# Optimization experiments

Measured on AMD Instinct MI355X. Metric: run time of the kernel, lower is better.

## Reference

```python
import jax, jax.numpy as jnp
import numpy as np

B, C, H, W = 4, 256, 64, 64
TOPK = 3
RAT_S = 0.05  # rat_s passed in Corr.forward


def _zero_window_mask(h, w, rat_s=RAT_S):
    # mask[m, i, j] = 1 - gaussian centered at pixel m=(m//w, m%w); sigma=(h*rat_s, w*rat_s)
    sr, sc = h * rat_s, w * rat_s
    r = jnp.arange(h, dtype=jnp.float32)
    c = jnp.arange(w, dtype=jnp.float32)
    cent_r = jnp.repeat(r, w)  # [hw]
    cent_c = jnp.tile(c, h)    # [hw]
    g = (jnp.exp(-((r[None, :, None] - cent_r[:, None, None]) ** 2) / (2.0 * sr * sr))
         * jnp.exp(-((c[None, None, :] - cent_c[:, None, None]) ** 2) / (2.0 * sc * sc)))
    return (1.0 - g).reshape(h * w, h * w)


def setup_inputs() -> dict:
    key = jax.random.key(0)
    x = jax.random.normal(key, (B, C, H, W), dtype=jnp.float32)
    alpha = jnp.asarray(5.0, dtype=jnp.float32)  # learned scalar nn.Parameter
    return {"x": x, "alpha": alpha}


def reference(x, alpha):
    b, c, h, w = x.shape
    # F.normalize(x, p=2, dim=-3): L2-normalize channels with eps clamp
    nrm = jnp.linalg.norm(x, axis=1, keepdims=True)
    xn = x / jnp.maximum(nrm, 1e-12)
    xf = xn.reshape(b, c, h * w)
    # correlation GEMM: [b, hw, hw]
    aff = jnp.einsum('bcm,bcn->bmn', xf, xf)
    aff = aff * _zero_window_mask(h, w)[None]
    s = aff * alpha
    xc = jax.nn.softmax(s, axis=-1) * jax.nn.softmax(s, axis=-2)
    # topk over the source-pixel dim (dim=-3 of [b, hw, h, w])
    xc = xc.reshape(b, h * w, h, w).transpose(0, 2, 3, 1)  # [b, h, w, hw]
    val, _ = jax.lax.top_k(xc, TOPK)                        # [b, h, w, k]
    return val.transpose(0, 3, 1, 2)                        # [b, k, h, w]
```

## Files before the change

kernel.cpp:

```cpp
#include <hip/hip_runtime.h>
#include <hip/hip_bf16.h>


#define HW 4096
#define CDIM 256
#define INV2S2 0.048828125f
#define NEGINF -1e30f
#define NTILE 528

typedef __bf16 bf16;
typedef _Float16 f16;
typedef __attribute__((ext_vector_type(8))) __bf16 bf16x8;
typedef __attribute__((ext_vector_type(4))) _Float16 f16x4;
typedef __attribute__((ext_vector_type(4))) float f32x4;

#define GAS __attribute__((address_space(1)))
#define LAS __attribute__((address_space(3)))

__device__ __forceinline__ void ins3(float v, float& t0, float& t1, float& t2) {
    float n0 = fmaxf(t0, v);
    float n1 = __builtin_amdgcn_fmed3f(t0, t1, v);
    float n2 = __builtin_amdgcn_fmed3f(t1, t2, v);
    t0 = n0; t1 = n1; t2 = n2;
}

__device__ __forceinline__ void decode_tri(int t, int& mt, int& nt) {
    int m = (int)((sqrtf(8.f * (float)t + 1.f) - 1.f) * 0.5f);
    while ((m + 1) * (m + 2) / 2 <= t) ++m;
    while (m * (m + 1) / 2 > t) --m;
    mt = m;
    nt = t - m * (m + 1) / 2;
}

__global__ __launch_bounds__(256) void corr_norm(const float* __restrict__ x,
                                                 bf16* __restrict__ xnT) {
    __shared__ float red[4][64];
    __shared__ float invn[64];
    __shared__ __align__(16) bf16 T[64][264];
    int tid = threadIdx.x;
    int pl = tid & 63, cg = tid >> 6;
    int P0 = blockIdx.x * 64;
    int P = P0 + pl;
    int b = P >> 12;
    int pix = P & 4095;
    const float* xb = x + ((size_t)(b * CDIM + cg * 64) << 12) + pix;
    float v[64];
    float ss = 0.f;
#pragma unroll
    for (int j = 0; j < 64; ++j) {
        v[j] = xb[(size_t)j << 12];
        ss += v[j] * v[j];
    }
    red[cg][pl] = ss;
    __syncthreads();
    if (tid < 64) {
        float s = red[0][tid] + red[1][tid] + red[2][tid] + red[3][tid];
        invn[tid] = 1.0f / fmaxf(sqrtf(s), 1e-12f);
    }
    __syncthreads();
    float inv = invn[pl];
#pragma unroll
    for (int j0 = 0; j0 < 64; j0 += 8) {
        bf16x8 pk;
#pragma unroll
        for (int j = 0; j < 8; ++j) pk[j] = (bf16)(v[j0 + j] * inv);
        *(bf16x8*)(&T[pl][cg * 64 + j0]) = pk;
    }
    __syncthreads();
#pragma unroll
    for (int it = 0; it < 8; ++it) {
        int p = it * 8 + (tid >> 5);
        int k = tid & 31;
        bf16x8 val = *(const bf16x8*)(&T[p][k * 8]);
        *(bf16x8*)(xnT + (size_t)(P0 + p) * CDIM + k * 8) = val;
    }
}

__device__ __forceinline__ void gemm_tile(const bf16* __restrict__ xb, int mbase, int nbase,
                                          bf16* As, bf16* Bs, f32x4 (&acc)[4][4]) {
    const int tid = threadIdx.x;
    const int wave = tid >> 6;
    const int lane = tid & 63;
    const int wm = wave >> 1, wn = wave & 1;
    const int l15 = lane & 15, quad = lane >> 4;
#pragma unroll
    for (int mi = 0; mi < 4; ++mi)
#pragma unroll
        for (int ni = 0; ni < 4; ++ni) acc[mi][ni] = (f32x4)0.f;

    auto issue = [&](int kk, int buf) {
#pragma unroll
        for (int r = 0; r < 2; ++r) {
            int idx = r * 256 + tid;
            int prow = idx >> 2;
            int sub = ((idx & 3) - (prow >> 1)) & 3;
            const bf16* gA = xb + ((size_t)(mbase + prow) << 8) + kk * 32 + (sub << 3);
            const bf16* gB = xb + ((size_t)(nbase + prow) << 8) + kk * 32 + (sub << 3);
            bf16* lA = As + buf * 4096 + ((r * 4 + wave) << 9);
            bf16* lB = Bs + buf * 4096 + ((r * 4 + wave) << 9);
            __builtin_amdgcn_global_load_lds((const GAS void*)gA, (LAS void*)lA, 16, 0, 0);
            __builtin_amdgcn_global_load_lds((const GAS void*)gB, (LAS void*)lB, 16, 0, 0);
        }
    };
    issue(0, 0);
    const int rslot = ((quad + (l15 >> 1)) & 3) * 8;
#pragma unroll
    for (int kk = 0; kk < 8; ++kk) {
        __syncthreads();
        if (kk < 7) issue(kk + 1, (kk + 1) & 1);
        int buf = kk & 1;
        bf16x8 af[4], bfr[4];
#pragma unroll
        for (int i = 0; i < 4; ++i) {
            af[i]  = *(const bf16x8*)(As + buf * 4096 + (wm * 64 + i * 16 + l15) * 32 + rslot);
            bfr[i] = *(const bf16x8*)(Bs + buf * 4096 + (wn * 64 + i * 16 + l15) * 32 + rslot);
        }
#pragma unroll
        for (int mi = 0; mi < 4; ++mi)
#pragma unroll
            for (int ni = 0; ni < 4; ++ni)
                acc[mi][ni] = __builtin_amdgcn_mfma_f32_16x16x32_bf16(af[mi], bfr[ni],
                                                                      acc[mi][ni], 0, 0, 0);
    }
}

__device__ __forceinline__ void build_ext(float* extw, int lane, int adr, float scale) {
    float fr2 = (float)(adr * adr);
#pragma unroll
    for (int h = 0; h < 2; ++h) {
        int j = lane + h * 64;
        float d = (float)(j - 63);
        extw[j] = scale * (1.f - __expf(-(fr2 + d * d) * INV2S2));
    }
}

__device__ __forceinline__ void load_etab(const float* extw_wave, int quad, int l15,
                                          float (&e)[7][4]) {
    const float* p = extw_wave + 63 + quad * 4 - l15;
#pragma unroll
    for (int dm = 0; dm < 7; ++dm)
#pragma unroll
        for (int r = 0; r < 4; ++r) e[dm][r] = p[(dm - 3) * 16 + r];
}

__global__ __launch_bounds__(256) void corr_rowsum(const bf16* __restrict__ xnT,
                                                   const float* __restrict__ alpha_p,
                                                   float* __restrict__ rpart,
                                                   f16* __restrict__ sbuf,
                                                   int store_s2) {
    __shared__ __align__(16) bf16 SH[16384];
    bf16* As = SH;
    bf16* Bs = SH + 8192;
    int tid = threadIdx.x;
    int lin = blockIdx.x;
    int xcd = lin & 7;
    int b = xcd >> 1;
    int t = ((lin >> 3) << 1) + (xcd & 1);
    int mt, nt;
    decode_tri(t, mt, nt);
    int mbase = mt * 128, nbase = nt * 128;
    int wave = tid >> 6, lane = tid & 63;
    int wm = wave >> 1, wn = wave & 1, l15 = lane & 15, quad = lane >> 4;
    int rowi = (mbase + wm * 64) >> 6;
    int coli = (nbase + wn * 64) >> 6;
    int adr = rowi - coli; if (adr < 0) adr = -adr;
    float alpha = alpha_p[0];

    f32x4 acc[4][4];
    gemm_tile(xnT + ((size_t)b << 20), mbase, nbase, As, Bs, acc);

    float* F = (float*)SH;
    float* ext  = F;
    float* rbuf = F + 512;
    float* cbuf = F + 768;
    build_ext(ext + wave * 128, lane, adr, alpha);
    float e[7][4];
    load_etab(ext + wave * 128, quad, l15, e);

    const size_t tb = (size_t)(b * NTILE + t) * 16384;
    float colpart[4] = {0.f, 0.f, 0.f, 0.f};
#pragma unroll
    for (int mi = 0; mi < 4; ++mi) {
#pragma unroll
        for (int r = 0; r < 4; ++r) {
            float ssum = 0.f;
            float sv[4];
#pragma unroll
            for (int ni = 0; ni < 4; ++ni) {
                float s = e[mi - ni + 3][r] * acc[mi][ni][r];
                sv[ni] = s;
                float ev = __expf(s);
                ssum += ev;
                colpart[ni] += ev;
            }
            if (store_s2) {
                f16x4 pk;
#pragma unroll
                for (int ni = 0; ni < 4; ++ni) pk[ni] = (f16)(sv[ni] + sv[ni]);
                *(f16x4*)(sbuf + tb + (mi * 4 + r) * 1024 + tid * 4) = pk;
            }
            ssum += __shfl_xor(ssum, 1);
            ssum += __shfl_xor(ssum, 2);
            ssum += __shfl_xor(ssum, 4);
            ssum += __shfl_xor(ssum, 8);
            if (l15 == 0) rbuf[wn * 128 + wm * 64 + mi * 16 + quad * 4 + r] = ssum;
        }
    }
#pragma unroll
    for (int ni = 0; ni < 4; ++ni) {
        float c = colpart[ni];
        c += __shfl_xor(c, 16);
        c += __shfl_xor(c, 32);
        if (quad == 0) cbuf[wm * 128 + wn * 64 + ni * 16 + l15] = c;
    }
    __syncthreads();
    if (tid < 128) {
        rpart[(size_t)((b * 32 + mt) * 32 + nt) * 128 + tid] = rbuf[tid] + rbuf[128 + tid];
    } else if (mt != nt) {
        int j = tid - 128;
        rpart[(size_t)((b * 32 + nt) * 32 + mt) * 128 + j] = cbuf[j] + cbuf[128 + j];
    }
}

__global__ __launch_bounds__(256) void corr_recip(const float* __restrict__ rpart,
                                                  float* __restrict__ ism,
                                                  float* __restrict__ lsm) {
    int i = blockIdx.x * 256 + threadIdx.x;
    if (i >= 4 * HW) return;
    int b = i >> 12, gr = i & 4095, s = gr >> 7, j = gr & 127;
    const float* base = rpart + (size_t)((b * 32 + s) * 32) * 128 + j;
    float sum = 0.f;
#pragma unroll
    for (int sl = 0; sl < 32; ++sl) sum += base[sl * 128];
    ism[i] = 1.0f / sum;
    lsm[i] = -__logf(sum);
}

__device__ __forceinline__ void topk_epilogue(int b, int mt, int nt,
                                              const float (&s2f)[16][4],
                                              const float (&lr)[4][4], const float (&lc)[4],
                                              float* mbuf, float* rtop,
                                              float* __restrict__ wtop,
                                              int tid, int wm, int wn, int l15, int quad) {
#pragma unroll
    for (int ni = 0; ni < 4; ++ni) {
        float t0 = NEGINF, t1 = NEGINF, t2 = NEGINF;
#pragma unroll
        for (int mi = 0; mi < 4; ++mi) {
#pragma unroll
            for (int r = 0; r < 4; ++r) {
                float key = s2f[mi * 4 + r][ni] + lr[mi][r];
                ins3(key, t0, t1, t2);
            }
        }
#pragma unroll
        for (int d = 16; d <= 32; d <<= 1) {
            float s0 = __shfl_xor(t0, d);
            float s1 = __shfl_xor(t1, d);
            float s2 = __shfl_xor(t2, d);
            ins3(s0, t0, t1, t2);
            ins3(s1, t0, t1, t2);
            ins3(s2, t0, t1, t2);
        }
        if (quad == 0) {
            int cl = wn * 64 + ni * 16 + l15;
            mbuf[(wm * 128 + cl) * 3 + 0] = t0;
            mbuf[(wm * 128 + cl) * 3 + 1] = t1;
            mbuf[(wm * 128 + cl) * 3 + 2] = t2;
        }
    }
    __syncthreads();
    if (mt != nt) {
#pragma unroll
        for (int mi = 0; mi < 4; ++mi) {
#pragma unroll
            for (int r = 0; r < 4; ++r) {
                float u0 = NEGINF, u1 = NEGINF, u2 = NEGINF;
#pragma unroll
                for (int ni = 0; ni < 4; ++ni) {
                    float key = s2f[mi * 4 + r][ni] + lc[ni];
                    ins3(key, u0, u1, u2);
                }
                {
                    float s0 = __shfl_xor(u0, 8);
                    float s1 = __shfl_xor(u1, 8);
                    float s2 = __shfl_xor(u2, 8);
                    ins3(s0, u0, u1, u2);
                    ins3(s1, u0, u1, u2);
                    ins3(s2, u0, u1, u2);
                }
                if (l15 < 8) {
                    int row = wm * 64 + mi * 16 + quad * 4 + r;
                    int slot = wn * 8 + l15;
                    float* q = rtop + row * 51 + slot * 3;
                    q[0] = u0; q[1] = u1; q[2] = u2;
                }
            }
        }
    }
    __syncthreads();
    if (tid < 128) {
        float t0 = mbuf[tid * 3], t1 = mbuf[tid * 3 + 1], t2 = mbuf[tid * 3 + 2];
        ins3(mbuf[(128 + tid) * 3 + 0], t0, t1, t2);
        ins3(mbuf[(128 + tid) * 3 + 1], t0, t1, t2);
        ins3(mbuf[(128 + tid) * 3 + 2], t0, t1, t2);
        size_t o = ((size_t)((b * 32 + nt) * 32 + mt) * 128 + tid) * 3;
        wtop[o] = t0;
        wtop[o + 1] = t1;
        wtop[o + 2] = t2;
        if (mt != nt) {
            float v0 = NEGINF, v1 = NEGINF, v2 = NEGINF;
            const float* q = rtop + tid * 51;
#pragma unroll
            for (int sl = 0; sl < 16; ++sl) {
                ins3(q[sl * 3 + 0], v0, v1, v2);
                ins3(q[sl * 3 + 1], v0, v1, v2);
                ins3(q[sl * 3 + 2], v0, v1, v2);
            }
            size_t o2 = ((size_t)((b * 32 + mt) * 32 + nt) * 128 + tid) * 3;
            wtop[o2] = v0;
            wtop[o2 + 1] = v1;
            wtop[o2 + 2] = v2;
        }
    }
}

__global__ __launch_bounds__(256) void corr_topsel(const f16* __restrict__ sbuf,
                                                   const float* __restrict__ lsm,
                                                   float* __restrict__ wtop) {
    __shared__ float FS[7296];
    float* mbuf = FS;
    float* rtop = FS + 768;
    int tid = threadIdx.x;
    int lin = blockIdx.x;
    int xcd = lin & 7;
    int b = xcd >> 1;
    int t = ((lin >> 3) << 1) + (xcd & 1);
    int mt, nt;
    decode_tri(t, mt, nt);
    int mbase = mt * 128, nbase = nt * 128;
    int wave = tid >> 6, lane = tid & 63;
    int wm = wave >> 1, wn = wave & 1, l15 = lane & 15, quad = lane >> 4;

    const size_t tb = (size_t)(b * NTILE + t) * 16384;
    float s2f[16][4];
#pragma unroll
    for (int k = 0; k < 16; ++k) {
        f16x4 hv = *(const f16x4*)(sbuf + tb + k * 1024 + tid * 4);
#pragma unroll
        for (int ni = 0; ni < 4; ++ni) s2f[k][ni] = (float)hv[ni];
    }
    float lr[4][4];
#pragma unroll
    for (int mi = 0; mi < 4; ++mi)
#pragma unroll
        for (int r = 0; r < 4; ++r)
            lr[mi][r] = lsm[(b << 12) + mbase + wm * 64 + mi * 16 + quad * 4 + r];
    float lc[4];
#pragma unroll
    for (int ni = 0; ni < 4; ++ni)
        lc[ni] = lsm[(b << 12) + nbase + wn * 64 + ni * 16 + l15];

    topk_epilogue(b, mt, nt, s2f, lr, lc, mbuf, rtop, wtop, tid, wm, wn, l15, quad);
}

__global__ __launch_bounds__(256) void corr_topk(const bf16* __restrict__ xnT,
                                                 const float* __restrict__ alpha_p,
                                                 const float* __restrict__ lsm,
                                                 float* __restrict__ wtop) {
    __shared__ __align__(16) bf16 SH[16384];
    bf16* As = SH;
    bf16* Bs = SH + 8192;
    int tid = threadIdx.x;
    int lin = blockIdx.x;
    int xcd = lin & 7;
    int b = xcd >> 1;
    int t = ((lin >> 3) << 1) + (xcd & 1);
    int mt, nt;
    decode_tri(t, mt, nt);
    int mbase = mt * 128, nbase = nt * 128;
    int wave = tid >> 6, lane = tid & 63;
    int wm = wave >> 1, wn = wave & 1, l15 = lane & 15, quad = lane >> 4;
    int rowi = (mbase + wm * 64) >> 6;
    int coli = (nbase + wn * 64) >> 6;
    int adr = rowi - coli; if (adr < 0) adr = -adr;
    float a2 = 2.0f * alpha_p[0];

    f32x4 acc[4][4];
    gemm_tile(xnT + ((size_t)b << 20), mbase, nbase, As, Bs, acc);

    float* F = (float*)SH;
    float* ext  = F;
    float* mbuf = F + 512;
    float* rtop = F + 1280;
    build_ext(ext + wave * 128, lane, adr, a2);
    float e[7][4];
    load_etab(ext + wave * 128, quad, l15, e);

    float s2f[16][4];
#pragma unroll
    for (int mi = 0; mi < 4; ++mi)
#pragma unroll
        for (int r = 0; r < 4; ++r)
#pragma unroll
            for (int ni = 0; ni < 4; ++ni)
                s2f[mi * 4 + r][ni] = e[mi - ni + 3][r] * acc[mi][ni][r];
    float lr[4][4];
#pragma unroll
    for (int mi = 0; mi < 4; ++mi)
#pragma unroll
        for (int r = 0; r < 4; ++r)
            lr[mi][r] = lsm[(b << 12) + mbase + wm * 64 + mi * 16 + quad * 4 + r];
    float lc[4];
#pragma unroll
    for (int ni = 0; ni < 4; ++ni)
        lc[ni] = lsm[(b << 12) + nbase + wn * 64 + ni * 16 + l15];

    __syncthreads();
    topk_epilogue(b, mt, nt, s2f, lr, lc, mbuf, rtop, wtop, tid, wm, wn, l15, quad);
}

__global__ __launch_bounds__(256) void corr_merge(const float* __restrict__ wtop,
                                                  const float* __restrict__ ism,
                                                  float* __restrict__ out) {
    int idx = blockIdx.x * 256 + threadIdx.x;
    if (idx >= 4 * HW) return;
    int b = idx >> 12, col = idx & 4095;
    int strip = col >> 7, j = col & 127;
    const float* base = wtop + ((size_t)((b * 32 + strip) * 32) * 128 + j) * 3;
    float t0 = NEGINF, t1 = NEGINF, t2 = NEGINF;
    for (int sl = 0; sl < 32; ++sl) {
        const float* q = base + (size_t)sl * 128 * 3;
        ins3(q[0], t0, t1, t2);
        ins3(q[1], t0, t1, t2);
        ins3(q[2], t0, t1, t2);
    }
    float ismc = ism[idx];
    out[((b * 3 + 0) << 12) + col] = __expf(t0) * ismc;
    out[((b * 3 + 1) << 12) + col] = __expf(t1) * ismc;
    out[((b * 3 + 2) << 12) + col] = __expf(t2) * ismc;
}

extern "C" void kernel_launch(void* const* d_in, const int* in_sizes, int n_in,
                              void* d_out, int out_size, void* d_ws, size_t ws_size,
                              hipStream_t stream) {
    const float* x = (const float*)d_in[0];
    const float* alpha = (const float*)d_in[1];
    float* out = (float*)d_out;
    char* ws = (char*)d_ws;
    bf16* xnT = (bf16*)ws;
    float* ism = (float*)(ws + (8u << 20));
    float* lsm = (float*)(ws + (8u << 20) + (64u << 10));
    float* rpart = (float*)(ws + (8u << 20) + (128u << 10));
    float* wtop  = (float*)(ws + (8u << 20) + (128u << 10));
    f16* sbuf = (f16*)(ws + (8u << 20) + (128u << 10) + (6u << 20));
    size_t need = (8u << 20) + (128u << 10) + (6u << 20) + (size_t)4 * NTILE * 16384 * 2;
    int fast = (ws_size >= need);

    corr_norm<<<256, 256, 0, stream>>>(x, xnT);
    corr_rowsum<<<NTILE * 4, 256, 0, stream>>>(xnT, alpha, rpart, sbuf, fast);
    corr_recip<<<64, 256, 0, stream>>>(rpart, ism, lsm);
    if (fast)
        corr_topsel<<<NTILE * 4, 256, 0, stream>>>(sbuf, lsm, wtop);
    else
        corr_topk<<<NTILE * 4, 256, 0, stream>>>(xnT, alpha, lsm, wtop);
    corr_merge<<<64, 256, 0, stream>>>(wtop, ism, out);
}
```

Baseline: 140.3 us.

## Load GEMM operands directly from global into registers, dropping LDS staging

Replaces the LDS-staged, double-buffered GEMM tile (global_load_lds plus a barrier per k-step) with per-lane direct global loads into registers, double-buffered across k-steps. This removes the shared-memory traffic and the eight block barriers per tile, and shrinks the kernels' LDS footprint, which may allow higher occupancy. In exchange, each operand row is fetched from global/L2 by several waves without reuse through LDS, and each lane issues strided 16-byte loads, which may raise cache traffic and expose more load latency.

Result: slower. 176.3 us (+25.7%).

```diff
diff --git a/kernel.cpp b/kernel.cpp
--- a/kernel.cpp
+++ b/kernel.cpp
@@ -76,8 +76,8 @@
     }
 }
 
-__device__ __forceinline__ void gemm_tile(const bf16* __restrict__ xb, int mbase, int nbase,
-                                          bf16* As, bf16* Bs, f32x4 (&acc)[4][4]) {
+__device__ __forceinline__ void gemm_direct(const bf16* __restrict__ xb, int mbase, int nbase,
+                                            f32x4 (&acc)[4][4]) {
     const int tid = threadIdx.x;
     const int wave = tid >> 6;
     const int lane = tid & 63;
@@ -88,38 +88,30 @@
 #pragma unroll
         for (int ni = 0; ni < 4; ++ni) acc[mi][ni] = (f32x4)0.f;
 
-    auto issue = [&](int kk, int buf) {
-#pragma unroll
-        for (int r = 0; r < 2; ++r) {
-            int idx = r * 256 + tid;
-            int prow = idx >> 2;
-            int sub = ((idx & 3) - (prow >> 1)) & 3;
-            const bf16* gA = xb + ((size_t)(mbase + prow) << 8) + kk * 32 + (sub << 3);
-            const bf16* gB = xb + ((size_t)(nbase + prow) << 8) + kk * 32 + (sub << 3);
-            bf16* lA = As + buf * 4096 + ((r * 4 + wave) << 9);
-            bf16* lB = Bs + buf * 4096 + ((r * 4 + wave) << 9);
-            __builtin_amdgcn_global_load_lds((const GAS void*)gA, (LAS void*)lA, 16, 0, 0);
-            __builtin_amdgcn_global_load_lds((const GAS void*)gB, (LAS void*)lB, 16, 0, 0);
-        }
-    };
-    issue(0, 0);
-    const int rslot = ((quad + (l15 >> 1)) & 3) * 8;
+    const bf16* pa = xb + ((size_t)(mbase + wm * 64 + l15) << 8) + (quad << 3);
+    const bf16* pb = xb + ((size_t)(nbase + wn * 64 + l15) << 8) + (quad << 3);
+
+    bf16x8 af[2][4], bq[2][4];
+#pragma unroll
+    for (int i = 0; i < 4; ++i) {
+        af[0][i] = *(const bf16x8*)(pa + (i << 12));
+        bq[0][i] = *(const bf16x8*)(pb + (i << 12));
+    }
 #pragma unroll
     for (int kk = 0; kk < 8; ++kk) {
-        __syncthreads();
-        if (kk < 7) issue(kk + 1, (kk + 1) & 1);
-        int buf = kk & 1;
-        bf16x8 af[4], bfr[4];
-#pragma unroll
-        for (int i = 0; i < 4; ++i) {
-            af[i]  = *(const bf16x8*)(As + buf * 4096 + (wm * 64 + i * 16 + l15) * 32 + rslot);
-            bfr[i] = *(const bf16x8*)(Bs + buf * 4096 + (wn * 64 + i * 16 + l15) * 32 + rslot);
+        const int cur = kk & 1, nxt = cur ^ 1;
+        if (kk < 7) {
+#pragma unroll
+            for (int i = 0; i < 4; ++i) {
+                af[nxt][i] = *(const bf16x8*)(pa + (i << 12) + ((kk + 1) << 5));
+                bq[nxt][i] = *(const bf16x8*)(pb + (i << 12) + ((kk + 1) << 5));
+            }
         }
 #pragma unroll
         for (int mi = 0; mi < 4; ++mi)
 #pragma unroll
             for (int ni = 0; ni < 4; ++ni)
-                acc[mi][ni] = __builtin_amdgcn_mfma_f32_16x16x32_bf16(af[mi], bfr[ni],
+                acc[mi][ni] = __builtin_amdgcn_mfma_f32_16x16x32_bf16(af[cur][mi], bq[cur][ni],
                                                                       acc[mi][ni], 0, 0, 0);
     }
 }
@@ -148,9 +140,7 @@
                                                    float* __restrict__ rpart,
                                                    f16* __restrict__ sbuf,
                                                    int store_s2) {
-    __shared__ __align__(16) bf16 SH[16384];
-    bf16* As = SH;
-    bf16* Bs = SH + 8192;
+    __shared__ float F[1024];
     int tid = threadIdx.x;
     int lin = blockIdx.x;
     int xcd = lin & 7;
@@ -167,9 +157,8 @@
     float alpha = alpha_p[0];
 
     f32x4 acc[4][4];
-    gemm_tile(xnT + ((size_t)b << 20), mbase, nbase, As, Bs, acc);
-
-    float* F = (float*)SH;
+    gemm_direct(xnT + ((size_t)b << 20), mbase, nbase, acc);
+
     float* ext  = F;
     float* rbuf = F + 512;
     float* cbuf = F + 768;
@@ -368,9 +357,10 @@
                                                  const float* __restrict__ alpha_p,
                                                  const float* __restrict__ lsm,
                                                  float* __restrict__ wtop) {
-    __shared__ __align__(16) bf16 SH[16384];
-    bf16* As = SH;
-    bf16* Bs = SH + 8192;
+    __shared__ float FS[7808];
+    float* ext  = FS;
+    float* mbuf = FS + 512;
+    float* rtop = FS + 1280;
     int tid = threadIdx.x;
     int lin = blockIdx.x;
     int xcd = lin & 7;
@@ -387,12 +377,8 @@
     float a2 = 2.0f * alpha_p[0];
 
     f32x4 acc[4][4];
-    gemm_tile(xnT + ((size_t)b << 20), mbase, nbase, As, Bs, acc);
-
-    float* F = (float*)SH;
-    float* ext  = F;
-    float* mbuf = F + 512;
-    float* rtop = F + 1280;
+    gemm_direct(xnT + ((size_t)b << 20), mbase, nbase, acc);
+
     build_ext(ext + wave * 128, lane, adr, a2);
     float e[7][4];
     load_etab(ext + wave * 128, quad, l15, e);
```

## Process two tiles per rowsum block, prefetching the next tile, and use exp2

Applied to the files above, without the earlier changes.

The rowsum kernel now handles two triangular tiles per block and launches half as many blocks. The first k-slice of the second tile is loaded while the first tile's exp and reduction epilogue runs. To make that safe, the epilogue scratch moves into its own shared array instead of reusing the GEMM buffers. Separately, log2(e) is folded into alpha so the kernels use native exp2 and log2 instead of exp and log, with the recip and merge kernels changed to match. The costs are extra LDS per block and fewer blocks in flight, which could reduce latency hiding.

Result: slower. 149.2 us (+6.4%).

```diff
diff --git a/kernel.cpp b/kernel.cpp
--- a/kernel.cpp
+++ b/kernel.cpp
@@ -1,5 +1,6 @@
 #include <hip/hip_runtime.h>
 #include <hip/hip_bf16.h>
+#include <math.h>
 
 
 #define HW 4096
@@ -7,6 +8,17 @@
 #define INV2S2 0.048828125f
 #define NEGINF -1e30f
 #define NTILE 528
+#define LOG2E 1.4426950408889634f
+
+#if defined(__has_builtin)
+#  if __has_builtin(__builtin_amdgcn_exp2f)
+#    define EXP2F(x) __builtin_amdgcn_exp2f(x)
+#  else
+#    define EXP2F(x) exp2f(x)
+#  endif
+#else
+#  define EXP2F(x) exp2f(x)
+#endif
 
 typedef __bf16 bf16;
 typedef _Float16 f16;
@@ -76,19 +88,50 @@
     }
 }
 
-__device__ __forceinline__ void gemm_tile(const bf16* __restrict__ xb, int mbase, int nbase,
-                                          bf16* As, bf16* Bs, f32x4 (&acc)[4][4]) {
-    const int tid = threadIdx.x;
-    const int wave = tid >> 6;
-    const int lane = tid & 63;
-    const int wm = wave >> 1, wn = wave & 1;
-    const int l15 = lane & 15, quad = lane >> 4;
-#pragma unroll
-    for (int mi = 0; mi < 4; ++mi)
-#pragma unroll
-        for (int ni = 0; ni < 4; ++ni) acc[mi][ni] = (f32x4)0.f;
-
-    auto issue = [&](int kk, int buf) {
+__device__ __forceinline__ void build_ext(float* extw, int lane, int adr, float scale) {
+    float fr2 = (float)(adr * adr);
+#pragma unroll
+    for (int h = 0; h < 2; ++h) {
+        int j = lane + h * 64;
+        float d = (float)(j - 63);
+        extw[j] = scale * (1.f - __expf(-(fr2 + d * d) * INV2S2));
+    }
+}
+
+__device__ __forceinline__ void load_etab(const float* extw_wave, int quad, int l15,
+                                          float (&e)[7][4]) {
+    const float* p = extw_wave + 63 + quad * 4 - l15;
+#pragma unroll
+    for (int dm = 0; dm < 7; ++dm)
+#pragma unroll
+        for (int r = 0; r < 4; ++r) e[dm][r] = p[(dm - 3) * 16 + r];
+}
+
+__global__ __launch_bounds__(256) void corr_rowsum(const bf16* __restrict__ xnT,
+                                                   const float* __restrict__ alpha_p,
+                                                   float* __restrict__ rpart,
+                                                   f16* __restrict__ sbuf,
+                                                   int store_s2) {
+    __shared__ __align__(16) bf16 SH[16384];
+    __shared__ float F[1024];
+    bf16* As = SH;
+    bf16* Bs = SH + 8192;
+    int tid = threadIdx.x;
+    int lin = blockIdx.x;
+    int xcd = lin & 7;
+    int b = xcd >> 1;
+    int pr = ((lin >> 3) << 1) + (xcd & 1);
+    int wave = tid >> 6, lane = tid & 63;
+    int wm = wave >> 1, wn = wave & 1, l15 = lane & 15, quad = lane >> 4;
+    float alpha2 = alpha_p[0] * LOG2E;
+    const bf16* xb = xnT + ((size_t)b << 20);
+    const int rslot = ((quad + (l15 >> 1)) & 3) * 8;
+
+    int mt0, nt0, mt1, nt1;
+    decode_tri(2 * pr, mt0, nt0);
+    decode_tri(2 * pr + 1, mt1, nt1);
+
+    auto issue = [&](int mbase, int nbase, int kk, int buf) {
 #pragma unroll
         for (int r = 0; r < 2; ++r) {
             int idx = r * 256 + tid;
@@ -102,123 +145,96 @@
             __builtin_amdgcn_global_load_lds((const GAS void*)gB, (LAS void*)lB, 16, 0, 0);
         }
     };
-    issue(0, 0);
-    const int rslot = ((quad + (l15 >> 1)) & 3) * 8;
-#pragma unroll
-    for (int kk = 0; kk < 8; ++kk) {
+
+    issue(mt0 * 128, nt0 * 128, 0, 0);
+
+    for (int tile = 0; tile < 2; ++tile) {
+        const int mt = tile ? mt1 : mt0;
+        const int nt = tile ? nt1 : nt0;
+        const int t = 2 * pr + tile;
+        const int mbase = mt * 128, nbase = nt * 128;
+
+        f32x4 acc[4][4];
+#pragma unroll
+        for (int mi = 0; mi < 4; ++mi)
+#pragma unroll
+            for (int ni = 0; ni < 4; ++ni) acc[mi][ni] = (f32x4)0.f;
+
+#pragma unroll
+        for (int kk = 0; kk < 8; ++kk) {
+            __syncthreads();
+            if (kk < 7)
+                issue(mbase, nbase, kk + 1, (kk + 1) & 1);
+            else if (tile == 0)
+                issue(mt1 * 128, nt1 * 128, 0, 0);
+            int buf = kk & 1;
+            bf16x8 af[4], bfr[4];
+#pragma unroll
+            for (int i = 0; i < 4; ++i) {
+                af[i]  = *(const bf16x8*)(As + buf * 4096 + (wm * 64 + i * 16 + l15) * 32 + rslot);
+                bfr[i] = *(const bf16x8*)(Bs + buf * 4096 + (wn * 64 + i * 16 + l15) * 32 + rslot);
+            }
+#pragma unroll
+            for (int mi = 0; mi < 4; ++mi)
+#pragma unroll
+                for (int ni = 0; ni < 4; ++ni)
+                    acc[mi][ni] = __builtin_amdgcn_mfma_f32_16x16x32_bf16(af[mi], bfr[ni],
+                                                                          acc[mi][ni], 0, 0, 0);
+        }
+
+        int rowi = (mbase + wm * 64) >> 6;
+        int coli = (nbase + wn * 64) >> 6;
+        int adr = rowi - coli; if (adr < 0) adr = -adr;
+        float* ext  = F;
+        float* rbuf = F + 512;
+        float* cbuf = F + 768;
+        build_ext(ext + wave * 128, lane, adr, alpha2);
+        float e[7][4];
+        load_etab(ext + wave * 128, quad, l15, e);
+
+        const size_t tb = (size_t)(b * NTILE + t) * 16384;
+        float colpart[4] = {0.f, 0.f, 0.f, 0.f};
+#pragma unroll
+        for (int mi = 0; mi < 4; ++mi) {
+#pragma unroll
+            for (int r = 0; r < 4; ++r) {
+                float ssum = 0.f;
+                float sv[4];
+#pragma unroll
+                for (int ni = 0; ni < 4; ++ni) {
+                    float p = e[mi - ni + 3][r] * acc[mi][ni][r];
+                    sv[ni] = p;
+                    float ev = EXP2F(p);
+                    ssum += ev;
+                    colpart[ni] += ev;
+                }
+                if (store_s2) {
+                    f16x4 pk;
+#pragma unroll
+                    for (int ni = 0; ni < 4; ++ni) pk[ni] = (f16)(sv[ni] + sv[ni]);
+                    *(f16x4*)(sbuf + tb + (mi * 4 + r) * 1024 + tid * 4) = pk;
+                }
+                ssum += __shfl_xor(ssum, 1);
+                ssum += __shfl_xor(ssum, 2);
+                ssum += __shfl_xor(ssum, 4);
+                ssum += __shfl_xor(ssum, 8);
+                if (l15 == 0) rbuf[wn * 128 + wm * 64 + mi * 16 + quad * 4 + r] = ssum;
+            }
+        }
+#pragma unroll
+        for (int ni = 0; ni < 4; ++ni) {
+            float c = colpart[ni];
+            c += __shfl_xor(c, 16);
+            c += __shfl_xor(c, 32);
+            if (quad == 0) cbuf[wm * 128 + wn * 64 + ni * 16 + l15] = c;
+        }
         __syncthreads();
-        if (kk < 7) issue(kk + 1, (kk + 1) & 1);
-        int buf = kk & 1;
-        bf16x8 af[4], bfr[4];
-#pragma unroll
-        for (int i = 0; i < 4; ++i) {
-            af[i]  = *(const bf16x8*)(As + buf * 4096 + (wm * 64 + i * 16 + l15) * 32 + rslot);
-            bfr[i] = *(const bf16x8*)(Bs + buf * 4096 + (wn * 64 + i * 16 + l15) * 32 + rslot);
-        }
-#pragma unroll
-        for (int mi = 0; mi < 4; ++mi)
-#pragma unroll
-            for (int ni = 0; ni < 4; ++ni)
-                acc[mi][ni] = __builtin_amdgcn_mfma_f32_16x16x32_bf16(af[mi], bfr[ni],
-                                                                      acc[mi][ni], 0, 0, 0);
-    }
-}
-
-__device__ __forceinline__ void build_ext(float* extw, int lane, int adr, float scale) {
-    float fr2 = (float)(adr * adr);
-#pragma unroll
-    for (int h = 0; h < 2; ++h) {
-        int j = lane + h * 64;
-        float d = (float)(j - 63);
-        extw[j] = scale * (1.f - __expf(-(fr2 + d * d) * INV2S2));
-    }
-}
-
-__device__ __forceinline__ void load_etab(const float* extw_wave, int quad, int l15,
-                                          float (&e)[7][4]) {
-    const float* p = extw_wave + 63 + quad * 4 - l15;
-#pragma unroll
-    for (int dm = 0; dm < 7; ++dm)
-#pragma unroll
-        for (int r = 0; r < 4; ++r) e[dm][r] = p[(dm - 3) * 16 + r];
-}
-
-__global__ __launch_bounds__(256) void corr_rowsum(const bf16* __restrict__ xnT,
-                                                   const float* __restrict__ alpha_p,
-                                                   float* __restrict__ rpart,
-                                                   f16* __restrict__ sbuf,
-                                                   int store_s2) {
-    __shared__ __align__(16) bf16 SH[16384];
-    bf16* As = SH;
-    bf16* Bs = SH + 8192;
-    int tid = threadIdx.x;
-    int lin = blockIdx.x;
-    int xcd = lin & 7;
-    int b = xcd >> 1;
-    int t = ((lin >> 3) << 1) + (xcd & 1);
-    int mt, nt;
-    decode_tri(t, mt, nt);
-    int mbase = mt * 128, nbase = nt * 128;
-    int wave = tid >> 6, lane = tid & 63;
-    int wm = wave >> 1, wn = wave & 1, l15 = lane & 15, quad = lane >> 4;
-    int rowi = (mbase + wm * 64) >> 6;
-    int coli = (nbase + wn * 64) >> 6;
-    int adr = rowi - coli; if (adr < 0) adr = -adr;
-    float alpha = alpha_p[0];
-
-    f32x4 acc[4][4];
-    gemm_tile(xnT + ((size_t)b << 20), mbase, nbase, As, Bs, acc);
-
-    float* F = (float*)SH;
-    float* ext  = F;
-    float* rbuf = F + 512;
-    float* cbuf = F + 768;
-    build_ext(ext + wave * 128, lane, adr, alpha);
-    float e[7][4];
-    load_etab(ext + wave * 128, quad, l15, e);
-
-    const size_t tb = (size_t)(b * NTILE + t) * 16384;
-    float colpart[4] = {0.f, 0.f, 0.f, 0.f};
-#pragma unroll
-    for (int mi = 0; mi < 4; ++mi) {
-#pragma unroll
-        for (int r = 0; r < 4; ++r) {
-            float ssum = 0.f;
-            float sv[4];
-#pragma unroll
-            for (int ni = 0; ni < 4; ++ni) {
-                float s = e[mi - ni + 3][r] * acc[mi][ni][r];
-                sv[ni] = s;
-                float ev = __expf(s);
-                ssum += ev;
-                colpart[ni] += ev;
-            }
-            if (store_s2) {
-                f16x4 pk;
-#pragma unroll
-                for (int ni = 0; ni < 4; ++ni) pk[ni] = (f16)(sv[ni] + sv[ni]);
-                *(f16x4*)(sbuf + tb + (mi * 4 + r) * 1024 + tid * 4) = pk;
-            }
-            ssum += __shfl_xor(ssum, 1);
-            ssum += __shfl_xor(ssum, 2);
-            ssum += __shfl_xor(ssum, 4);
-            ssum += __shfl_xor(ssum, 8);
-            if (l15 == 0) rbuf[wn * 128 + wm * 64 + mi * 16 + quad * 4 + r] = ssum;
-        }
-    }
-#pragma unroll
-    for (int ni = 0; ni < 4; ++ni) {
-        float c = colpart[ni];
-        c += __shfl_xor(c, 16);
-        c += __shfl_xor(c, 32);
-        if (quad == 0) cbuf[wm * 128 + wn * 64 + ni * 16 + l15] = c;
-    }
-    __syncthreads();
-    if (tid < 128) {
-        rpart[(size_t)((b * 32 + mt) * 32 + nt) * 128 + tid] = rbuf[tid] + rbuf[128 + tid];
-    } else if (mt != nt) {
-        int j = tid - 128;
-        rpart[(size_t)((b * 32 + nt) * 32 + mt) * 128 + j] = cbuf[j] + cbuf[128 + j];
+        if (tid < 128) {
+            rpart[(size_t)((b * 32 + mt) * 32 + nt) * 128 + tid] = rbuf[tid] + rbuf[128 + tid];
+        } else if (mt != nt) {
+            int j = tid - 128;
+            rpart[(size_t)((b * 32 + nt) * 32 + mt) * 128 + j] = cbuf[j] + cbuf[128 + j];
+        }
     }
 }
 
@@ -233,7 +249,7 @@
 #pragma unroll
     for (int sl = 0; sl < 32; ++sl) sum += base[sl * 128];
     ism[i] = 1.0f / sum;
-    lsm[i] = -__logf(sum);
+    lsm[i] = -log2f(sum);
 }
 
 __device__ __forceinline__ void topk_epilogue(int b, int mt, int nt,
@@ -384,15 +400,54 @@
     int rowi = (mbase + wm * 64) >> 6;
     int coli = (nbase + wn * 64) >> 6;
     int adr = rowi - coli; if (adr < 0) adr = -adr;
-    float a2 = 2.0f * alpha_p[0];
+    float a2 = 2.0f * alpha_p[0] * LOG2E;
+    const bf16* xb = xnT + ((size_t)b << 20);
+    const int rslot = ((quad + (l15 >> 1)) & 3) * 8;
+
+    auto issue = [&](int kk, int buf) {
+#pragma unroll
+        for (int r = 0; r < 2; ++r) {
+            int idx = r * 256 + tid;
+            int prow = idx >> 2;
+            int sub = ((idx & 3) - (prow >> 1)) & 3;
+            const bf16* gA = xb + ((size_t)(mbase + prow) << 8) + kk * 32 + (sub << 3);
+            const bf16* gB = xb + ((size_t)(nbase + prow) << 8) + kk * 32 + (sub << 3);
+            bf16* lA = As + buf * 4096 + ((r * 4 + wave) << 9);
+            bf16* lB = Bs + buf * 4096 + ((r * 4 + wave) << 9);
+            __builtin_amdgcn_global_load_lds((const GAS void*)gA, (LAS void*)lA, 16, 0, 0);
+            __builtin_amdgcn_global_load_lds((const GAS void*)gB, (LAS void*)lB, 16, 0, 0);
+        }
+    };
 
     f32x4 acc[4][4];
-    gemm_tile(xnT + ((size_t)b << 20), mbase, nbase, As, Bs, acc);
-
-    float* F = (float*)SH;
-    float* ext  = F;
-    float* mbuf = F + 512;
-    float* rtop = F + 1280;
+#pragma unroll
+    for (int mi = 0; mi < 4; ++mi)
+#pragma unroll
+        for (int ni = 0; ni < 4; ++ni) acc[mi][ni] = (f32x4)0.f;
+    issue(0, 0);
+#pragma unroll
+    for (int kk = 0; kk < 8; ++kk) {
+        __syncthreads();
+        if (kk < 7) issue(kk + 1, (kk + 1) & 1);
+        int buf = kk & 1;
+        bf16x8 af[4], bfr[4];
+#pragma unroll
+        for (int i = 0; i < 4; ++i) {
+            af[i]  = *(const bf16x8*)(As + buf * 4096 + (wm * 64 + i * 16 + l15) * 32 + rslot);
+            bfr[i] = *(const bf16x8*)(Bs + buf * 4096 + (wn * 64 + i * 16 + l15) * 32 + rslot);
+        }
+#pragma unroll
+        for (int mi = 0; mi < 4; ++mi)
+#pragma unroll
+            for (int ni = 0; ni < 4; ++ni)
+                acc[mi][ni] = __builtin_amdgcn_mfma_f32_16x16x32_bf16(af[mi], bfr[ni],
+                                                                      acc[mi][ni], 0, 0, 0);
+    }
+
+    float* Fh = (float*)SH;
+    float* ext  = Fh;
+    float* mbuf = Fh + 512;
+    float* rtop = Fh + 1280;
     build_ext(ext + wave * 128, lane, adr, a2);
     float e[7][4];
     load_etab(ext + wave * 128, quad, l15, e);
@@ -436,9 +491,9 @@
         ins3(q[2], t0, t1, t2);
     }
     float ismc = ism[idx];
-    out[((b * 3 + 0) << 12) + col] = __expf(t0) * ismc;
-    out[((b * 3 + 1) << 12) + col] = __expf(t1) * ismc;
-    out[((b * 3 + 2) << 12) + col] = __expf(t2) * ismc;
+    out[((b * 3 + 0) << 12) + col] = EXP2F(t0) * ismc;
+    out[((b * 3 + 1) << 12) + col] = EXP2F(t1) * ismc;
+    out[((b * 3 + 2) << 12) + col] = EXP2F(t2) * ismc;
 }
 
 extern "C" void kernel_launch(void* const* d_in, const int* in_sizes, int n_in,
@@ -458,7 +513,7 @@
     int fast = (ws_size >= need);
 
     corr_norm<<<256, 256, 0, stream>>>(x, xnT);
-    corr_rowsum<<<NTILE * 4, 256, 0, stream>>>(xnT, alpha, rpart, sbuf, fast);
+    corr_rowsum<<<NTILE * 2, 256, 0, stream>>>(xnT, alpha, rpart, sbuf, fast);
     corr_recip<<<64, 256, 0, stream>>>(rpart, ism, lsm);
     if (fast)
         corr_topsel<<<NTILE * 4, 256, 0, stream>>>(sbuf, lsm, wtop);
```
